# Optimization experiments

Measured on AMD Instinct MI355X. Metric: run time of the kernel, lower is better.

Reference implementation:

```python
import jax, jax.numpy as jnp
import numpy as np
import math

N_HEAD = 16
ROPE_BASE = 10000.0


def _rope_as_in_source(x):
    """Faithful replication of RotaryPositionalEmbeddings.forward applied to
    x of shape [B, H, T, hd] (called after transpose in the source, so
    seq_len = x.size(1) = H: angles are indexed by head index, not position)."""
    B, H, T, hd = x.shape
    theta = 1.0 / (ROPE_BASE ** (jnp.arange(0, hd, 2, dtype=jnp.float32) / hd))  # [hd/2]
    ang = jnp.arange(H, dtype=jnp.float32)[:, None] * theta[None, :]  # [H, hd/2]
    cos = jnp.cos(ang)[None, :, None, :]  # [1, H, 1, hd/2]
    sin = jnp.sin(ang)[None, :, None, :]
    xr = x.reshape(B, H, T, hd // 2, 2)
    out = jnp.stack([
        xr[..., 0] * cos - xr[..., 1] * sin,
        xr[..., 1] * cos + xr[..., 0] * sin,
    ], axis=-1)
    return out.reshape(B, H, T, hd)


def setup_inputs() -> dict:
    key = jax.random.key(0)
    ks = jax.random.split(key, 5)
    B, T, C = 2, 2048, 1024
    s = 0.02
    return {
        "x": jax.random.normal(ks[0], (B, T, C), dtype=jnp.float32),
        "W_attn": jax.random.normal(ks[1], (C, 3 * C), dtype=jnp.float32) * s,
        "b_attn": jnp.zeros((3 * C,), dtype=jnp.float32),
        "W_proj": jax.random.normal(ks[2], (C, C), dtype=jnp.float32) * s,
        "b_proj": jnp.zeros((C,), dtype=jnp.float32),
    }


def reference(x, W_attn, b_attn, W_proj, b_proj):
    B, T, C = x.shape
    H = N_HEAD
    hd = C // H
    qkv = x @ W_attn + b_attn  # [B, T, 3C]
    q, k, v = jnp.split(qkv, 3, axis=2)
    # [B, T, H, hd] -> [B, H, T, hd]
    q = q.reshape(B, T, H, hd).transpose(0, 2, 1, 3)
    k = k.reshape(B, T, H, hd).transpose(0, 2, 1, 3)
    v = v.reshape(B, T, H, hd).transpose(0, 2, 1, 3)
    q = _rope_as_in_source(q)
    k = _rope_as_in_source(k)
    att = jnp.einsum("bhqd,bhkd->bhqk", q, k) * (1.0 / math.sqrt(hd))
    causal = jnp.tril(jnp.ones((T, T), dtype=bool))
    att = jnp.where(causal[None, None, :, :], att, -jnp.inf)
    att = jax.nn.softmax(att, axis=-1)
    y = jnp.einsum("bhqk,bhkd->bhqd", att, v)  # [B, H, T, hd]
    y = y.transpose(0, 2, 1, 3).reshape(B, T, C)
    return y @ W_proj + b_proj
```

## Files before the change

kernel.cpp:

```cpp
#include <hip/hip_runtime.h>

typedef __attribute__((ext_vector_type(8))) short bf16x8;
typedef __attribute__((ext_vector_type(4))) float f32x4;
typedef __attribute__((ext_vector_type(4))) unsigned int uint4v;
typedef unsigned short ushort_t;

#define BB 2
#define TT 2048
#define CC 1024
#define HH 16
#define HD 64
#define MM (BB * TT)
#define N3C (3 * CC)
#define KD 1024
#define NTILES 32

__device__ __forceinline__ ushort_t f2b(float f) {
  unsigned u = __builtin_bit_cast(unsigned, f);
  u += 0x7fffu + ((u >> 16) & 1u);
  return (ushort_t)(u >> 16);
}

__device__ __forceinline__ unsigned pack2rne(float a, float b) {
  return (unsigned)f2b(a) | ((unsigned)f2b(b) << 16);
}

__device__ __forceinline__ unsigned pack2bf(float a, float b) {
  unsigned ua = (__builtin_bit_cast(unsigned, a) + 0x8000u) >> 16;
  unsigned ub = (__builtin_bit_cast(unsigned, b) + 0x8000u) & 0xffff0000u;
  return ua | ub;
}

__device__ __forceinline__ float fexp2(float x) {
#if __has_builtin(__builtin_amdgcn_exp2f)
  return __builtin_amdgcn_exp2f(x);
#else
  return __expf(x * 0.6931471805599453f);
#endif
}

__device__ __forceinline__ f32x4 mfma16(bf16x8 a, bf16x8 b, f32x4 c) {
  return __builtin_amdgcn_mfma_f32_16x16x32_bf16(a, b, c, 0, 0, 0);
}

__device__ __forceinline__ void load_lds16(const void* g, void* l) {
  __builtin_amdgcn_global_load_lds((const __attribute__((address_space(1))) void*)g,
                                   (__attribute__((address_space(3))) void*)l, 16, 0, 0);
}

__global__ __launch_bounds__(256) void prep(const float* __restrict__ x,
                                            const float* __restrict__ Wa,
                                            const float* __restrict__ Wp,
                                            ushort_t* __restrict__ xb,
                                            ushort_t* __restrict__ wat,
                                            ushort_t* __restrict__ wpt) {
  const int blk = blockIdx.x, tid = threadIdx.x;
  if (blk < 4096) {
    int i = blk * 256 + tid;
    const float4 v = ((const float4*)x)[i];
    typedef __attribute__((ext_vector_type(4))) ushort_t us4;
    us4 r;
    r.x = f2b(v.x); r.y = f2b(v.y); r.z = f2b(v.z); r.w = f2b(v.w);
    ((us4*)xb)[i] = r;
    return;
  }
  __shared__ ushort_t tile[32][33];
  const float* W; ushort_t* Wt; int R, Nc, n0, r0;
  if (blk < 7168) {
    int tb = blk - 4096;
    W = Wa; Wt = wat; R = CC; Nc = N3C;
    n0 = (tb % 96) * 32; r0 = (tb / 96) * 32;
  } else {
    int tb = blk - 7168;
    W = Wp; Wt = wpt; R = CC; Nc = CC;
    n0 = (tb & 31) * 32; r0 = (tb >> 5) * 32;
  }
  const int c = tid & 31, rr = tid >> 5;
#pragma unroll
  for (int i = 0; i < 4; ++i) {
    int r = rr + i * 8;
    tile[r][c] = f2b(W[(size_t)(r0 + r) * Nc + n0 + c]);
  }
  __syncthreads();
#pragma unroll
  for (int i = 0; i < 4; ++i) {
    int r = rr + i * 8;
    Wt[(size_t)(n0 + r) * R + r0 + c] = tile[c][r];
  }
}

__global__ __launch_bounds__(512, 2) void qkv256(const ushort_t* __restrict__ A,
                                                 const ushort_t* __restrict__ Bt,
                                                 const float* __restrict__ bias,
                                                 ushort_t* __restrict__ qo,
                                                 ushort_t* __restrict__ ko,
                                                 ushort_t* __restrict__ vto) {
  extern __shared__ ushort_t lds[];
  ushort_t* As = lds;
  ushort_t* Bs = lds + 32768;

  const int tid = threadIdx.x, lane = tid & 63, wave = tid >> 6;
  const int l15 = lane & 15, quad = lane >> 4;
  const int wm = (wave >> 2) * 128, wn = (wave & 3) * 64;
  const int m0 = blockIdx.y * 256, n0 = blockIdx.x * 256;

  const int lin0 = tid, lin1 = 512 + tid;
  const int rw0 = lin0 >> 2, c0 = (lin0 & 3) ^ (rw0 & 3);
  const int rw1 = lin1 >> 2, c1 = (lin1 & 3) ^ (rw1 & 3);
  const ushort_t* sA0 = A + (size_t)(m0 + rw0) * KD + c0 * 8;
  const ushort_t* sA1 = A + (size_t)(m0 + rw1) * KD + c1 * 8;
  const ushort_t* sB0 = Bt + (size_t)(n0 + rw0) * KD + c0 * 8;
  const ushort_t* sB1 = Bt + (size_t)(n0 + rw1) * KD + c1 * 8;
  ushort_t* dA0 = As + lin0 * 8;
  ushort_t* dA1 = As + lin1 * 8;
  ushort_t* dB0 = Bs + lin0 * 8;
  ushort_t* dB1 = Bs + lin1 * 8;

  auto stage = [&](int t) {
    const int bo = (t & 3) * 8192;
    const size_t k8 = (size_t)t * 32;
    load_lds16(sA0 + k8, dA0 + bo);
    load_lds16(sA1 + k8, dA1 + bo);
    load_lds16(sB0 + k8, dB0 + bo);
    load_lds16(sB1 + k8, dB1 + bo);
  };

  const int swc = (quad ^ (l15 & 3)) * 8;
  const int rdA = (wm + l15) * 32 + swc;
  const int rdB = (wn + l15) * 32 + swc;

  f32x4 acc[8][4] = {};

  stage(0); stage(1); stage(2);

  for (int t = 0; t < NTILES; ++t) {
    if (t < NTILES - 2)       asm volatile("s_waitcnt vmcnt(8)" ::: "memory");
    else if (t == NTILES - 2) asm volatile("s_waitcnt vmcnt(4)" ::: "memory");
    else                      asm volatile("s_waitcnt vmcnt(0)" ::: "memory");
    __builtin_amdgcn_s_barrier();
    if (t + 3 < NTILES) stage(t + 3);

    const ushort_t* Ap = As + (t & 3) * 8192;
    const ushort_t* Bp = Bs + (t & 3) * 8192;
    bf16x8 af[8], bfr[4];
#pragma unroll
    for (int j = 0; j < 4; ++j) bfr[j] = *(const bf16x8*)&Bp[rdB + j * 512];
#pragma unroll
    for (int i = 0; i < 8; ++i) af[i] = *(const bf16x8*)&Ap[rdA + i * 512];

    __builtin_amdgcn_s_setprio(1);
#pragma unroll
    for (int i = 0; i < 8; ++i)
#pragma unroll
      for (int j = 0; j < 4; ++j)
        acc[i][j] = mfma16(af[i], bfr[j], acc[i][j]);
    __builtin_amdgcn_s_setprio(0);
  }

  float bv[4];
#pragma unroll
  for (int j = 0; j < 4; ++j) bv[j] = bias[n0 + wn + j * 16 + l15];

  const int h8 = l15 >> 3, j8l = l15 & 7;
  const int t0 = (m0 + wm) & 2047, b = (m0 + wm) >> 11;
  const int gsec = (n0 + wn) >> 10, h = ((n0 + wn) & 1023) >> 6;
  const int bh = b * HH + h;
  if (gsec < 2) {
    ushort_t* dst = (gsec == 0 ? qo + ((size_t)bh * 128 + (t0 >> 4)) * 1024
                               : ko + ((size_t)bh * 32 + (t0 >> 6)) * 4096)
                    + h8 * 128 + quad * 32 + j8l;
#pragma unroll
    for (int i = 0; i < 8; ++i)
#pragma unroll
      for (int j = 0; j < 4; ++j)
#pragma unroll
        for (int r = 0; r < 4; ++r)
          dst[i * 1024 + (j >> 1) * 512 + (j & 1) * 256 + r * 8] =
              f2b(acc[i][j][r] + bv[j]);
  } else {
    ushort_t* dst = vto + ((size_t)bh * 32 + (t0 >> 6)) * 4096 + quad * 128 + l15 * 8;
#pragma unroll
    for (int j = 0; j < 4; ++j)
#pragma unroll
      for (int i = 0; i < 8; ++i) {
        uint2 u;
        u.x = pack2rne(acc[i][j][0] + bv[j], acc[i][j][1] + bv[j]);
        u.y = pack2rne(acc[i][j][2] + bv[j], acc[i][j][3] + bv[j]);
        const int il = i & 3;
        *(uint2*)&dst[(i >> 2) * 4096 + j * 1024 + (il >> 1) * 512 + (il & 1) * 4] = u;
      }
  }
}

template <int EPI, int NT>
__global__ __launch_bounds__(256) void gemm_bt(const ushort_t* __restrict__ A,
                                               const ushort_t* __restrict__ Bt,
                                               const float* __restrict__ bias,
                                               ushort_t* __restrict__ qo,
                                               ushort_t* __restrict__ ko,
                                               ushort_t* __restrict__ vto,
                                               float* __restrict__ outp,
                                               int N, int K) {
  constexpr int NJ = NT / 32;
  __shared__ __align__(16) ushort_t As[128 * 64];
  __shared__ __align__(16) ushort_t Bs[NT * 64];
  const int tid = threadIdx.x, lane = tid & 63, wave = tid >> 6;
  const int l15 = lane & 15, quad = lane >> 4;
  const int wm = (wave >> 1) * 64, wn = (wave & 1) * (NT / 2);
  const int m0 = blockIdx.y * 128, n0 = blockIdx.x * NT;

  f32x4 acc[4][NJ] = {};
  for (int k0 = 0; k0 < K; k0 += 64) {
    __syncthreads();
#pragma unroll
    for (int p = 0; p < 4; ++p) {
      int d16 = p * 256 + tid;
      int pan = d16 >> 9, rem = d16 & 511, row = rem >> 2, cc = rem & 3;
      load_lds16(&A[(size_t)(m0 + row) * K + k0 + pan * 32 + cc * 8], &As[d16 * 8]);
    }
#pragma unroll
    for (int p = 0; p < NT / 32; ++p) {
      int d16 = p * 256 + tid;
      int pan = d16 / (NT * 4), rem = d16 % (NT * 4), row = rem >> 2, cc = rem & 3;
      load_lds16(&Bt[(size_t)(n0 + row) * K + k0 + pan * 32 + cc * 8], &Bs[d16 * 8]);
    }
    __syncthreads();
#pragma unroll
    for (int pan = 0; pan < 2; ++pan) {
      const ushort_t* Ap = &As[pan * 4096];
      const ushort_t* Bp = &Bs[pan * (NT * 32)];
      bf16x8 af[4], bfr[NJ];
#pragma unroll
      for (int i = 0; i < 4; ++i)
        af[i] = *(const bf16x8*)&Ap[(wm + i * 16 + l15) * 32 + quad * 8];
#pragma unroll
      for (int j = 0; j < NJ; ++j)
        bfr[j] = *(const bf16x8*)&Bp[(wn + j * 16 + l15) * 32 + quad * 8];
#pragma unroll
      for (int i = 0; i < 4; ++i)
#pragma unroll
        for (int j = 0; j < NJ; ++j)
          acc[i][j] = mfma16(af[i], bfr[j], acc[i][j]);
    }
  }

  float bv[NJ];
#pragma unroll
  for (int j = 0; j < NJ; ++j) bv[j] = bias[n0 + wn + j * 16 + l15];

  if (EPI == 1) {
#pragma unroll
    for (int i = 0; i < 4; ++i)
#pragma unroll
      for (int r = 0; r < 4; ++r) {
        float* rp = outp + (size_t)(m0 + wm + i * 16 + quad * 4 + r) * N + n0 + wn + l15;
#pragma unroll
        for (int j = 0; j < NJ; ++j) rp[j * 16] = acc[i][j][r] + bv[j];
      }
  }
}

__global__ __launch_bounds__(256) void attn_kernel(const ushort_t* __restrict__ Qf,
                                                   const ushort_t* __restrict__ Kf,
                                                   const ushort_t* __restrict__ Vf,
                                                   ushort_t* __restrict__ y) {
  __shared__ __align__(16) float red[2][2176];
  const int tid = threadIdx.x, lane = tid & 63, wave = tid >> 6;
  const int l15 = lane & 15, quad = lane >> 4;
  const int idx = blockIdx.x;
  const int xcd = idx & 7, j = idx >> 3;
  const int bh = xcd * 4 + (j & 3);
  const int g = 63 - (j >> 2);
  const int qs = g * 32;
  const int nk = (qs + 95) >> 6;

  const float SCL = 0.125f * 1.4426950408889634f;

  const ushort_t* qbase = Qf + (((size_t)bh * 128 + (qs >> 4)) * 2 * 64 + lane) * 8;
  bf16x8 qf[2][2];
#pragma unroll
  for (int st = 0; st < 2; ++st)
#pragma unroll
    for (int dh = 0; dh < 2; ++dh)
      qf[st][dh] = *(const bf16x8*)(qbase + (st * 2 + dh) * 512);

  f32x4 o[2][4] = {};
  float l_r[2] = {0.f, 0.f};

  for (int it = wave; it < nk; it += 4) {
    const bool diag = (it == nk - 1);
    const size_t tb = ((size_t)bh * 32 + it) * 4096 + (size_t)lane * 8;
    bf16x8 kf[4][2], vf[4][2];
#pragma unroll
    for (int ng = 0; ng < 4; ++ng)
#pragma unroll
      for (int dh = 0; dh < 2; ++dh)
        kf[ng][dh] = *(const bf16x8*)(Kf + tb + (ng * 2 + dh) * 512);
#pragma unroll
    for (int dg = 0; dg < 4; ++dg)
#pragma unroll
      for (int h = 0; h < 2; ++h)
        vf[dg][h] = *(const bf16x8*)(Vf + tb + (dg * 2 + h) * 512);

#pragma unroll
    for (int st = 0; st < 2; ++st) {
      f32x4 s[4];
      __builtin_amdgcn_s_setprio(1);
#pragma unroll
      for (int ng = 0; ng < 4; ++ng) {
        f32x4 z = {};
        z = mfma16(kf[ng][0], qf[st][0], z);
        z = mfma16(kf[ng][1], qf[st][1], z);
        s[ng] = z;
      }
      __builtin_amdgcn_s_setprio(0);
      float p[4][4];
      const int qg = qs + st * 16 + l15;
#pragma unroll
      for (int ng = 0; ng < 4; ++ng)
#pragma unroll
        for (int r = 0; r < 4; ++r) {
          float pv = fexp2(s[ng][r] * SCL);
          if (diag) {
            int kg = it * 64 + ng * 16 + quad * 4 + r;
            pv = (kg > qg) ? 0.f : pv;
          }
          p[ng][r] = pv;
          l_r[st] += pv;
        }
      union { uint4v u; bf16x8 v; } pk0, pk1;
      pk0.u[0] = pack2bf(p[0][0], p[0][1]); pk0.u[1] = pack2bf(p[0][2], p[0][3]);
      pk0.u[2] = pack2bf(p[1][0], p[1][1]); pk0.u[3] = pack2bf(p[1][2], p[1][3]);
      pk1.u[0] = pack2bf(p[2][0], p[2][1]); pk1.u[1] = pack2bf(p[2][2], p[2][3]);
      pk1.u[2] = pack2bf(p[3][0], p[3][1]); pk1.u[3] = pack2bf(p[3][2], p[3][3]);
      __builtin_amdgcn_s_setprio(1);
#pragma unroll
      for (int dg = 0; dg < 4; ++dg) {
        o[st][dg] = mfma16(vf[dg][0], pk0.v, o[st][dg]);
        o[st][dg] = mfma16(vf[dg][1], pk1.v, o[st][dg]);
      }
      __builtin_amdgcn_s_setprio(0);
    }
  }

  auto dump = [&](float* buf) {
#pragma unroll
    for (int st = 0; st < 2; ++st)
#pragma unroll
      for (int dg = 0; dg < 4; ++dg)
        *(f32x4*)&buf[(st * 4 + dg) * 256 + lane * 4] = o[st][dg];
    buf[2048 + lane * 2 + 0] = l_r[0];
    buf[2048 + lane * 2 + 1] = l_r[1];
  };
  auto merge = [&](const float* buf) {
#pragma unroll
    for (int st = 0; st < 2; ++st)
#pragma unroll
      for (int dg = 0; dg < 4; ++dg)
        o[st][dg] += *(const f32x4*)&buf[(st * 4 + dg) * 256 + lane * 4];
    l_r[0] += buf[2048 + lane * 2 + 0];
    l_r[1] += buf[2048 + lane * 2 + 1];
  };
  if (wave == 1) dump(red[0]);
  if (wave == 3) dump(red[1]);
  __syncthreads();
  if (wave == 0) merge(red[0]);
  if (wave == 2) merge(red[1]);
  __syncthreads();
  if (wave == 2) dump(red[0]);
  __syncthreads();
  if (wave == 0) {
    merge(red[0]);
    const int b = bh >> 4, h = bh & 15;
#pragma unroll
    for (int st = 0; st < 2; ++st) {
      float lf = l_r[st];
      lf += __shfl_xor(lf, 16);
      lf += __shfl_xor(lf, 32);
      const float inv = 1.0f / lf;
      const size_t row = (size_t)(b * TT + qs + st * 16 + l15) * CC;
#pragma unroll
      for (int dg = 0; dg < 4; ++dg) {
        uint2 u;
        u.x = pack2rne(o[st][dg][0] * inv, o[st][dg][1] * inv);
        u.y = pack2rne(o[st][dg][2] * inv, o[st][dg][3] * inv);
        *(uint2*)&y[row + h * HD + dg * 16 + quad * 4] = u;
      }
    }
  }
}

extern "C" void kernel_launch(void* const* d_in, const int* in_sizes, int n_in,
                              void* d_out, int out_size, void* d_ws, size_t ws_size,
                              hipStream_t stream) {
  const float* x  = (const float*)d_in[0];
  const float* Wa = (const float*)d_in[1];
  const float* ba = (const float*)d_in[2];
  const float* Wp = (const float*)d_in[3];
  const float* bp = (const float*)d_in[4];
  float* out = (float*)d_out;

  char* ws = (char*)d_ws;
  ushort_t* xb  = (ushort_t*)(ws + 0);
  ushort_t* wat = (ushort_t*)(ws + 8388608);
  ushort_t* wpt = (ushort_t*)(ws + 14680064);
  ushort_t* Qf  = (ushort_t*)(ws + 16777216);
  ushort_t* Kf  = (ushort_t*)(ws + 25165824);
  ushort_t* Vf  = (ushort_t*)(ws + 33554432);
  ushort_t* yb  = (ushort_t*)(ws + 41943040);

  static int attr_done = 0;
  if (!attr_done) {
    (void)hipFuncSetAttribute((const void*)qkv256,
                              hipFuncAttributeMaxDynamicSharedMemorySize, 131072);
    attr_done = 1;
  }

  prep<<<8192, 256, 0, stream>>>(x, Wa, Wp, xb, wat, wpt);

  qkv256<<<dim3(N3C / 256, MM / 256), 512, 131072, stream>>>(xb, wat, ba, Qf, Kf, Vf);

  attn_kernel<<<2048, 256, 0, stream>>>(Qf, Kf, Vf, yb);

  gemm_bt<1, 64><<<dim3(CC / 64, MM / 128), 256, 0, stream>>>(
      yb, wpt, bp, nullptr, nullptr, nullptr, out, CC, CC);
}
```

Measured before the change: 178.1 us.

## Restructure QKV GEMM mainloop into four-phase ping-pong schedule with staged half-tile loads

Rewrites the QKV GEMM K-loop to step 64 at a time over two double-buffered halves. Each step splits into four barrier-delimited phases that interleave LDS fragment reads, issue of the next half-tile global-to-LDS loads, and 16-MFMA clusters, using sched_barrier to pin the ordering. The aim is to overlap memory traffic with matrix math more finely and cut fragment register pressure, at the cost of many more block-wide barriers per iteration. It also drops the setprio hints around the MFMA clusters in the attention kernel.

```diff
diff --git a/kernel.cpp b/kernel.cpp
--- a/kernel.cpp
+++ b/kernel.cpp
@@ -13,7 +13,7 @@
 #define MM (BB * TT)
 #define N3C (3 * CC)
 #define KD 1024
-#define NTILES 32
+#define NT64 16
 
 __device__ __forceinline__ ushort_t f2b(float f) {
   unsigned u = __builtin_bit_cast(unsigned, f);
@@ -47,6 +47,10 @@
   __builtin_amdgcn_global_load_lds((const __attribute__((address_space(1))) void*)g,
                                    (__attribute__((address_space(3))) void*)l, 16, 0, 0);
 }
+
+#define BAR()   __builtin_amdgcn_s_barrier()
+#define SB0()   __builtin_amdgcn_sched_barrier(0)
+#define LGKM0() asm volatile("s_waitcnt lgkmcnt(0)" ::: "memory")
 
 __global__ __launch_bounds__(256) void prep(const float* __restrict__ x,
                                             const float* __restrict__ Wa,
@@ -104,25 +108,27 @@
   const int wm = (wave >> 2) * 128, wn = (wave & 3) * 64;
   const int m0 = blockIdx.y * 256, n0 = blockIdx.x * 256;
 
-  const int lin0 = tid, lin1 = 512 + tid;
-  const int rw0 = lin0 >> 2, c0 = (lin0 & 3) ^ (rw0 & 3);
-  const int rw1 = lin1 >> 2, c1 = (lin1 & 3) ^ (rw1 & 3);
-  const ushort_t* sA0 = A + (size_t)(m0 + rw0) * KD + c0 * 8;
-  const ushort_t* sA1 = A + (size_t)(m0 + rw1) * KD + c1 * 8;
-  const ushort_t* sB0 = Bt + (size_t)(n0 + rw0) * KD + c0 * 8;
-  const ushort_t* sB1 = Bt + (size_t)(n0 + rw1) * KD + c1 * 8;
-  ushort_t* dA0 = As + lin0 * 8;
-  ushort_t* dA1 = As + lin1 * 8;
-  ushort_t* dB0 = Bs + lin0 * 8;
-  ushort_t* dB1 = Bs + lin1 * 8;
-
-  auto stage = [&](int t) {
-    const int bo = (t & 3) * 8192;
-    const size_t k8 = (size_t)t * 32;
-    load_lds16(sA0 + k8, dA0 + bo);
-    load_lds16(sA1 + k8, dA1 + bo);
-    load_lds16(sB0 + k8, dB0 + bo);
-    load_lds16(sB1 + k8, dB1 + bo);
+  const int rw0 = tid >> 2, gc0 = (tid & 3) ^ (rw0 & 3);
+  const ushort_t* sA0 = A + (size_t)(m0 + rw0) * KD + gc0 * 8;
+  const ushort_t* sA1 = sA0 + (size_t)128 * KD;
+  const ushort_t* sB0 = Bt + (size_t)(n0 + rw0) * KD + gc0 * 8;
+  const ushort_t* sB1 = sB0 + (size_t)128 * KD;
+  ushort_t* dA0 = As + tid * 8;
+  ushort_t* dA1 = dA0 + 4096;
+  ushort_t* dB0 = Bs + tid * 8;
+  ushort_t* dB1 = dB0 + 4096;
+
+  auto stA = [&](int tau, int kh) {
+    const int so = ((tau & 1) * 2 + kh) * 8192;
+    const int ko2 = tau * 64 + kh * 32;
+    load_lds16(sA0 + ko2, dA0 + so);
+    load_lds16(sA1 + ko2, dA1 + so);
+  };
+  auto stB = [&](int tau, int kh) {
+    const int so = ((tau & 1) * 2 + kh) * 8192;
+    const int ko2 = tau * 64 + kh * 32;
+    load_lds16(sB0 + ko2, dB0 + so);
+    load_lds16(sB1 + ko2, dB1 + so);
   };
 
   const int swc = (quad ^ (l15 & 3)) * 8;
@@ -131,30 +137,81 @@
 
   f32x4 acc[8][4] = {};
 
-  stage(0); stage(1); stage(2);
-
-  for (int t = 0; t < NTILES; ++t) {
-    if (t < NTILES - 2)       asm volatile("s_waitcnt vmcnt(8)" ::: "memory");
-    else if (t == NTILES - 2) asm volatile("s_waitcnt vmcnt(4)" ::: "memory");
-    else                      asm volatile("s_waitcnt vmcnt(0)" ::: "memory");
-    __builtin_amdgcn_s_barrier();
-    if (t + 3 < NTILES) stage(t + 3);
-
-    const ushort_t* Ap = As + (t & 3) * 8192;
-    const ushort_t* Bp = Bs + (t & 3) * 8192;
-    bf16x8 af[8], bfr[4];
-#pragma unroll
-    for (int j = 0; j < 4; ++j) bfr[j] = *(const bf16x8*)&Bp[rdB + j * 512];
-#pragma unroll
-    for (int i = 0; i < 8; ++i) af[i] = *(const bf16x8*)&Ap[rdA + i * 512];
-
+  stB(0, 0); stA(0, 0); stB(0, 1); stA(0, 1);
+  stB(1, 0); stA(1, 0); stB(1, 1);
+  asm volatile("s_waitcnt vmcnt(6)" ::: "memory");
+  BAR();
+  SB0();
+
+  bf16x8 a[4], b0[4], b1[4];
+  for (int t = 0; t < NT64; ++t) {
+    const int par = t & 1;
+    const ushort_t* aK0 = As + par * 16384;
+    const ushort_t* aK1 = aK0 + 8192;
+    const ushort_t* bK0 = Bs + par * 16384;
+    const ushort_t* bK1 = bK0 + 8192;
+
+#pragma unroll
+    for (int j = 0; j < 4; ++j) b0[j] = *(const bf16x8*)&bK0[rdB + j * 512];
+#pragma unroll
+    for (int i = 0; i < 4; ++i) a[i] = *(const bf16x8*)&aK0[rdA + i * 512];
+    if (t + 1 < NT64) stA(t + 1, 1);
+    BAR();
+    LGKM0();
     __builtin_amdgcn_s_setprio(1);
 #pragma unroll
-    for (int i = 0; i < 8; ++i)
-#pragma unroll
-      for (int j = 0; j < 4; ++j)
-        acc[i][j] = mfma16(af[i], bfr[j], acc[i][j]);
+    for (int i = 0; i < 4; ++i)
+#pragma unroll
+      for (int j = 0; j < 4; ++j) acc[i][j] = mfma16(a[i], b0[j], acc[i][j]);
     __builtin_amdgcn_s_setprio(0);
+    BAR();
+    SB0();
+
+#pragma unroll
+    for (int i = 0; i < 4; ++i) a[i] = *(const bf16x8*)&aK0[rdA + (4 + i) * 512];
+    if (t + 2 < NT64) stB(t + 2, 0);
+    BAR();
+    LGKM0();
+    __builtin_amdgcn_s_setprio(1);
+#pragma unroll
+    for (int i = 0; i < 4; ++i)
+#pragma unroll
+      for (int j = 0; j < 4; ++j) acc[4 + i][j] = mfma16(a[i], b0[j], acc[4 + i][j]);
+    __builtin_amdgcn_s_setprio(0);
+    BAR();
+    SB0();
+
+#pragma unroll
+    for (int j = 0; j < 4; ++j) b1[j] = *(const bf16x8*)&bK1[rdB + j * 512];
+#pragma unroll
+    for (int i = 0; i < 4; ++i) a[i] = *(const bf16x8*)&aK1[rdA + i * 512];
+    if (t + 2 < NT64) stA(t + 2, 0);
+    BAR();
+    LGKM0();
+    __builtin_amdgcn_s_setprio(1);
+#pragma unroll
+    for (int i = 0; i < 4; ++i)
+#pragma unroll
+      for (int j = 0; j < 4; ++j) acc[i][j] = mfma16(a[i], b1[j], acc[i][j]);
+    __builtin_amdgcn_s_setprio(0);
+    BAR();
+    SB0();
+
+#pragma unroll
+    for (int i = 0; i < 4; ++i) a[i] = *(const bf16x8*)&aK1[rdA + (4 + i) * 512];
+    if (t + 2 < NT64) stB(t + 2, 1);
+    if (t < NT64 - 2)       { asm volatile("s_waitcnt vmcnt(6)" ::: "memory"); }
+    else if (t == NT64 - 2) { asm volatile("s_waitcnt vmcnt(0)" ::: "memory"); }
+    BAR();
+    LGKM0();
+    __builtin_amdgcn_s_setprio(1);
+#pragma unroll
+    for (int i = 0; i < 4; ++i)
+#pragma unroll
+      for (int j = 0; j < 4; ++j) acc[4 + i][j] = mfma16(a[i], b1[j], acc[4 + i][j]);
+    __builtin_amdgcn_s_setprio(0);
+    BAR();
+    SB0();
   }
 
   float bv[4];
@@ -305,7 +362,6 @@
 #pragma unroll
     for (int st = 0; st < 2; ++st) {
       f32x4 s[4];
-      __builtin_amdgcn_s_setprio(1);
 #pragma unroll
       for (int ng = 0; ng < 4; ++ng) {
         f32x4 z = {};
@@ -313,7 +369,6 @@
         z = mfma16(kf[ng][1], qf[st][1], z);
         s[ng] = z;
       }
-      __builtin_amdgcn_s_setprio(0);
       float p[4][4];
       const int qg = qs + st * 16 + l15;
 #pragma unroll
@@ -333,13 +388,11 @@
       pk0.u[2] = pack2bf(p[1][0], p[1][1]); pk0.u[3] = pack2bf(p[1][2], p[1][3]);
       pk1.u[0] = pack2bf(p[2][0], p[2][1]); pk1.u[1] = pack2bf(p[2][2], p[2][3]);
       pk1.u[2] = pack2bf(p[3][0], p[3][1]); pk1.u[3] = pack2bf(p[3][2], p[3][3]);
-      __builtin_amdgcn_s_setprio(1);
 #pragma unroll
       for (int dg = 0; dg < 4; ++dg) {
         o[st][dg] = mfma16(vf[dg][0], pk0.v, o[st][dg]);
         o[st][dg] = mfma16(vf[dg][1], pk1.v, o[st][dg]);
       }
-      __builtin_amdgcn_s_setprio(0);
     }
   }
 
```

New measurement: 175.9 us. Within noise of the previous version (-1.3%).
